# Kernel tuning notes

Hardware: AMD Instinct MI355X
Metric: run time of the kernel (lower is better)

The kernel has to match this reference:

```python
import jax, jax.numpy as jnp
import numpy as np

DIM = 512
HEADS = 8
DH = 64          # dim_head = 512 // 8
M = 256          # num_landmarks = 512 // 2
PINV_ITERS = 6
N_PATCH = 40000
IN_DIM = 1024
NUM_CLASSES = 2
GRID = 200       # ceil(sqrt(40000)) -> exact square, add_length = 0


def layernorm(x, w, b, eps=1e-5):
    mu = x.mean(-1, keepdims=True)
    var = ((x - mu) ** 2).mean(-1, keepdims=True)
    return (x - mu) * jax.lax.rsqrt(var + eps) * w + b


def moore_penrose_pinv(x, iters=PINV_ITERS):
    # lucidrains nystrom-attention iterative pseudoinverse
    ax = jnp.abs(x)
    z = jnp.swapaxes(x, -1, -2) / (jnp.max(ax.sum(-1)) * jnp.max(ax.sum(-2)))
    I = jnp.eye(x.shape[-1], dtype=x.dtype)
    for _ in range(iters):
        xz = x @ z
        z = 0.25 * z @ (13 * I - xz @ (15 * I - xz @ (7 * I - xz)))
    return z


def depthwise_conv2d(x, w, pad):
    # x: (B,C,H,W); w: (C,1,kh,kw) torch-style OIHW depthwise kernel
    return jax.lax.conv_general_dilated(
        x, w, (1, 1), [(pad[0], pad[0]), (pad[1], pad[1])],
        dimension_numbers=('NCHW', 'OIHW', 'NCHW'),
        feature_group_count=x.shape[1])


def nystrom_attention(x, qkv_w, out_w, out_b, res_w):
    b, n, _ = x.shape
    pad = (M - n % M) % M
    xp = jnp.pad(x, ((0, 0), (pad, 0), (0, 0)))   # pad at FRONT of sequence
    N = n + pad
    qkv = xp @ qkv_w                              # (b,N,3*h*d), no bias
    q, k, v = jnp.split(qkv, 3, axis=-1)
    to_heads = lambda t: t.reshape(b, N, HEADS, DH).transpose(0, 2, 1, 3)
    q, k, v = to_heads(q), to_heads(k), to_heads(v)
    q = q * (DH ** -0.5)
    l = N // M
    q_l = q.reshape(b, HEADS, M, l, DH).mean(axis=3)   # (b,h,m,d) landmarks
    k_l = k.reshape(b, HEADS, M, l, DH).mean(axis=3)
    attn1 = jax.nn.softmax(jnp.einsum('bhid,bhjd->bhij', q, k_l), axis=-1)   # (b,h,N,m)
    attn2 = jax.nn.softmax(jnp.einsum('bhid,bhjd->bhij', q_l, k_l), axis=-1)  # (b,h,m,m)
    attn3 = jax.nn.softmax(jnp.einsum('bhid,bhjd->bhij', q_l, k), axis=-1)   # (b,h,m,N)
    out = (attn1 @ moore_penrose_pinv(attn2)) @ (attn3 @ v)                   # (b,h,N,d)
    out = out + depthwise_conv2d(v, res_w, (16, 0))    # residual depthwise conv (kernel 33x1)
    out = out.transpose(0, 2, 1, 3).reshape(b, N, HEADS * DH)[:, -n:]
    return out @ out_w + out_b


def ppeg(x, w7, b7, w5, b5, w3, b3, H, W):
    B, _, C = x.shape
    cls_t, feat = x[:, :1], x[:, 1:]
    f = feat.transpose(0, 2, 1).reshape(B, C, H, W)
    y = (f
         + depthwise_conv2d(f, w7, (3, 3)) + b7[None, :, None, None]
         + depthwise_conv2d(f, w5, (2, 2)) + b5[None, :, None, None]
         + depthwise_conv2d(f, w3, (1, 1)) + b3[None, :, None, None])
    y = y.reshape(B, C, H * W).transpose(0, 2, 1)
    return jnp.concatenate([cls_t, y], axis=1)


def setup_inputs() -> dict:
    key = jax.random.key(0)
    ks = iter(jax.random.split(key, 32))
    r = lambda shape, s=0.02: jax.random.normal(next(ks), shape, dtype=jnp.float32) * s
    inp = {
        'x': jax.random.normal(next(ks), (1, N_PATCH, IN_DIM), dtype=jnp.float32),
        'fc1_w': r((IN_DIM, DIM)), 'fc1_b': jnp.zeros((DIM,), jnp.float32),
        'cls_token': r((1, 1, DIM), 1e-6),
        'l1_norm_w': jnp.ones((DIM,), jnp.float32), 'l1_norm_b': jnp.zeros((DIM,), jnp.float32),
        'l1_qkv_w': r((DIM, 3 * HEADS * DH)), 'l1_out_w': r((HEADS * DH, DIM)),
        'l1_out_b': jnp.zeros((DIM,), jnp.float32), 'l1_res_w': r((HEADS, 1, 33, 1)),
        'p7_w': r((DIM, 1, 7, 7)), 'p7_b': jnp.zeros((DIM,), jnp.float32),
        'p5_w': r((DIM, 1, 5, 5)), 'p5_b': jnp.zeros((DIM,), jnp.float32),
        'p3_w': r((DIM, 1, 3, 3)), 'p3_b': jnp.zeros((DIM,), jnp.float32),
        'l2_norm_w': jnp.ones((DIM,), jnp.float32), 'l2_norm_b': jnp.zeros((DIM,), jnp.float32),
        'l2_qkv_w': r((DIM, 3 * HEADS * DH)), 'l2_out_w': r((HEADS * DH, DIM)),
        'l2_out_b': jnp.zeros((DIM,), jnp.float32), 'l2_res_w': r((HEADS, 1, 33, 1)),
        'norm_w': jnp.ones((DIM,), jnp.float32), 'norm_b': jnp.zeros((DIM,), jnp.float32),
        'fc2_w': r((DIM, NUM_CLASSES)), 'fc2_b': jnp.zeros((NUM_CLASSES,), jnp.float32),
    }
    return inp


def reference(x, fc1_w, fc1_b, cls_token,
              l1_norm_w, l1_norm_b, l1_qkv_w, l1_out_w, l1_out_b, l1_res_w,
              p7_w, p7_b, p5_w, p5_b, p3_w, p3_b,
              l2_norm_w, l2_norm_b, l2_qkv_w, l2_out_w, l2_out_b, l2_res_w,
              norm_w, norm_b, fc2_w, fc2_b):
    # _fc1: Linear + ReLU (dropout inactive at eval)
    h = jax.nn.relu(x @ fc1_w + fc1_b)            # (1, 40000, 512)
    # 40000 = 200*200 -> add_length = 0, no square padding needed
    B = h.shape[0]
    h = jnp.concatenate([jnp.broadcast_to(cls_token, (B, 1, DIM)), h], axis=1)
    # layer1: pre-norm Nystrom attention with residual
    h = h + nystrom_attention(layernorm(h, l1_norm_w, l1_norm_b), l1_qkv_w, l1_out_w, l1_out_b, l1_res_w)
    # PPEG positional mixing on the 200x200 token grid
    h = ppeg(h, p7_w, p7_b, p5_w, p5_b, p3_w, p3_b, GRID, GRID)
    # layer2
    h = h + nystrom_attention(layernorm(h, l2_norm_w, l2_norm_b), l2_qkv_w, l2_out_w, l2_out_b, l2_res_w)
    h = layernorm(h, norm_w, norm_b)
    cls_out = h[:, 0]
    logits = cls_out @ fc2_w + fc2_b              # (1, num_classes)
    return logits
```

## Files before the change

### kernel.cpp

```cpp
#include <hip/hip_runtime.h>
#include <hip/hip_bf16.h>

#define DIMC   512
#define HEADS  8
#define DH     64
#define MLM    256
#define NPATCH 40000
#define NTOK   40001
#define PADF   191
#define NSEQ   40192
#define NSEQP  40224
#define LWIN   157
#define INDIM  1024
#define GRID   200
#define CHUNKS 64
#define PER    628

typedef _Float16 h8 __attribute__((ext_vector_type(8)));
typedef _Float16 h4 __attribute__((ext_vector_type(4)));
typedef float    f4 __attribute__((ext_vector_type(4)));
typedef float    f2 __attribute__((ext_vector_type(2)));

#define WAVE_LDS_FENCE() asm volatile("s_waitcnt lgkmcnt(0)" ::: "memory")

__device__ __forceinline__ void gl_lds(const _Float16* g, _Float16* l) {
  __builtin_amdgcn_global_load_lds(
      (const __attribute__((address_space(1))) void*)g,
      (__attribute__((address_space(3))) void*)l, 16, 0, 0);
}

template<int NW, bool ISMAX>
__device__ __forceinline__ float blkRed(float v, float* s) {
  #pragma unroll
  for (int o = 32; o; o >>= 1) {
    float t = __shfl_down(v, o, 64);
    v = ISMAX ? fmaxf(v, t) : v + t;
  }
  int lane = threadIdx.x & 63, w = threadIdx.x >> 6;
  __syncthreads();
  if (lane == 0) s[w] = v;
  __syncthreads();
  float r = s[0];
  #pragma unroll
  for (int i = 1; i < NW; i++) r = ISMAX ? fmaxf(r, s[i]) : r + s[i];
  return r;
}

__global__ __launch_bounds__(512)
void k_set_cls(const float* __restrict__ cls, float* __restrict__ h) {
  h[threadIdx.x] = cls[threadIdx.x];
}

__global__ __launch_bounds__(256)
void k_f32_to_f16(const float* __restrict__ in, _Float16* __restrict__ out) {
  int i = blockIdx.x * 256 + threadIdx.x;
  float4 v = ((const float4*)in)[i];
  h4 o = {(_Float16)v.x, (_Float16)v.y, (_Float16)v.z, (_Float16)v.w};
  *(h4*)(out + (size_t)i * 4) = o;
}

__global__ __launch_bounds__(256)
void k_zpad(_Float16* q16, _Float16* k16, _Float16* v16) {
  int idx = blockIdx.x * 256 + threadIdx.x;
  int h = idx >> 11, r = (idx >> 6) & 31, d = idx & 63;
  size_t a = ((size_t)h * NSEQP + NSEQ + r) * 64 + d;
  q16[a] = (_Float16)0.f; k16[a] = (_Float16)0.f; v16[a] = (_Float16)0.f;
}

__global__ __launch_bounds__(256)
void k_wt16(const float* __restrict__ B, _Float16* __restrict__ Bt, int K, int N)
{
  __shared__ float tile[32][33];
  int kb = blockIdx.x * 32, nb = blockIdx.y * 32;
  int x = threadIdx.x & 31, y0 = threadIdx.x >> 5;
  #pragma unroll
  for (int yy = y0; yy < 32; yy += 8)
    tile[yy][x] = B[(size_t)(kb + yy) * N + nb + x];
  __syncthreads();
  #pragma unroll
  for (int yy = y0; yy < 32; yy += 8)
    Bt[(size_t)(nb + yy) * K + kb + x] = (_Float16)tile[x][yy];
}

__global__ __launch_bounds__(256)
void k_gemm16(const _Float16* __restrict__ A, const _Float16* __restrict__ Bt,
              const float* __restrict__ bias, float* __restrict__ C,
              _Float16* __restrict__ q16, _Float16* __restrict__ k16, _Float16* __restrict__ v16,
              int Mr, int K, int N, int flags)
{
  __shared__ __attribute__((aligned(16))) _Float16 As[128 * 32];
  __shared__ __attribute__((aligned(16))) _Float16 Bs[128 * 32];
  int NT = N >> 7;
  int nwg = gridDim.x;
  int q8 = nwg >> 3, r8 = nwg & 7;
  int xcd = blockIdx.x & 7, sidx = blockIdx.x >> 3;
  int wgid = (xcd < r8) ? (xcd * (q8 + 1) + sidx)
                        : (r8 * (q8 + 1) + (xcd - r8) * q8 + sidx);
  int bm = (wgid / NT) * 128, bn = (wgid % NT) * 128;
  int t = threadIdx.x;
  int lane = t & 63, w = t >> 6;
  int wm = (w >> 1) * 64, wn = (w & 1) * 64;
  int r = lane & 15, q = lane >> 4;
  int sub = lane >> 2;
  int kq = (lane & 3) * 8;

  const f4 zero = {0.f, 0.f, 0.f, 0.f};
  f4 acc[4][4];
  #pragma unroll
  for (int mi = 0; mi < 4; mi++)
    #pragma unroll
    for (int nj = 0; nj < 4; nj++) acc[mi][nj] = zero;

  for (int k0 = 0; k0 < K; k0 += 32) {
    #pragma unroll
    for (int c = 0; c < 2; c++) {
      int rowA = (w * 2 + c) * 16 + sub;
      int gmA = bm + rowA; if (gmA > Mr - 1) gmA = Mr - 1;
      gl_lds(A  + (size_t)gmA * K + k0 + kq,          As + (w * 2 + c) * 512);
      gl_lds(Bt + (size_t)(bn + rowA) * K + k0 + kq,  Bs + (w * 2 + c) * 512);
    }
    __syncthreads();
    h8 af[4], bf[4];
    #pragma unroll
    for (int i = 0; i < 4; i++) {
      af[i] = *(const h8*)(As + (wm + i * 16 + r) * 32 + q * 8);
      bf[i] = *(const h8*)(Bs + (wn + i * 16 + r) * 32 + q * 8);
    }
    #pragma unroll
    for (int mi = 0; mi < 4; mi++)
      #pragma unroll
      for (int nj = 0; nj < 4; nj++)
        acc[mi][nj] = __builtin_amdgcn_mfma_f32_16x16x32_f16(bf[nj], af[mi], acc[mi][nj], 0, 0, 0);
    __syncthreads();
  }
  #pragma unroll
  for (int mi = 0; mi < 4; mi++) {
    int gm = bm + wm + mi * 16 + r;
    if (gm >= Mr) continue;
    #pragma unroll
    for (int nj = 0; nj < 4; nj++) {
      int gn = bn + wn + nj * 16 + q * 4;
      f4 v = acc[mi][nj];
      if (flags & 4) {
        int which = gn >> 9, hh = (gn >> 6) & 7, dd = gn & 63;
        _Float16* dst = (which == 0) ? q16 : (which == 1) ? k16 : v16;
        h4 o = {(_Float16)v[0], (_Float16)v[1], (_Float16)v[2], (_Float16)v[3]};
        *(h4*)(dst + ((size_t)hh * NSEQP + gm) * 64 + dd) = o;
      } else {
        if (bias) { f4 bv = *(const f4*)(bias + gn); v += bv; }
        float* cp = C + (size_t)gm * N + gn;
        if (flags & 2) { f4 cv = *(const f4*)cp; v += cv; }
        if (flags & 1) {
          v[0] = fmaxf(v[0], 0.f); v[1] = fmaxf(v[1], 0.f);
          v[2] = fmaxf(v[2], 0.f); v[3] = fmaxf(v[3], 0.f);
        }
        *(f4*)cp = v;
      }
    }
  }
}

__global__ __launch_bounds__(256)
void k_ln_pad(const float* __restrict__ h, const float* __restrict__ w,
              const float* __restrict__ b, _Float16* __restrict__ xln)
{
  __shared__ float sbuf[8];
  int t = blockIdx.x;
  int tid = threadIdx.x;
  _Float16* out = xln + (size_t)t * DIMC;
  if (t < PADF) { out[tid] = (_Float16)0.f; out[tid + 256] = (_Float16)0.f; return; }
  const float* row = h + (size_t)(t - PADF) * DIMC;
  float x0 = row[tid], x1 = row[tid + 256];
  float mu = blkRed<4,false>(x0 + x1, sbuf) * (1.f / 512.f);
  float d0 = x0 - mu, d1 = x1 - mu;
  float var = blkRed<4,false>(d0 * d0 + d1 * d1, sbuf) * (1.f / 512.f);
  float rstd = rsqrtf(var + 1e-5f);
  out[tid]       = (_Float16)(d0 * rstd * w[tid]       + b[tid]);
  out[tid + 256] = (_Float16)(d1 * rstd * w[tid + 256] + b[tid + 256]);
}

__global__ __launch_bounds__(256)
void k_vt(const _Float16* __restrict__ v16, _Float16* __restrict__ vt16)
{
  __shared__ _Float16 tl[64][72];
  int h = blockIdx.y;
  int t0 = blockIdx.x * 64;
  for (int c = threadIdx.x; c < 512; c += 256) {
    int row = c >> 3, ch = (c & 7) * 8;
    h8 v = {};
    if (t0 + row < NSEQP)
      v = *(const h8*)(v16 + ((size_t)h * NSEQP + t0 + row) * 64 + ch);
    *(h8*)&tl[row][ch] = v;
  }
  __syncthreads();
  int d = threadIdx.x & 63, tg = (threadIdx.x >> 6) * 16;
  if (t0 + tg < NSEQP) {
    _Float16 tmp[16];
    #pragma unroll
    for (int k = 0; k < 16; k++) tmp[k] = tl[tg + k][d];
    *(h8*)(vt16 + ((size_t)h * 64 + d) * NSEQP + t0 + tg)     = *(h8*)tmp;
    *(h8*)(vt16 + ((size_t)h * 64 + d) * NSEQP + t0 + tg + 8) = *(h8*)(tmp + 8);
  }
}

__global__ __launch_bounds__(256)
void k_landmarks(const _Float16* __restrict__ q16, const _Float16* __restrict__ k16,
                 float* __restrict__ ql, float* __restrict__ kl,
                 _Float16* __restrict__ ql16, _Float16* __restrict__ kl16)
{
  __shared__ float red[2][16][64];
  int h = blockIdx.x >> 8, i = blockIdx.x & 255;
  int jg = threadIdx.x >> 4, d4 = (threadIdx.x & 15) * 4;
  const _Float16* qb = q16 + ((size_t)h * NSEQP + i * LWIN) * 64;
  const _Float16* kb = k16 + ((size_t)h * NSEQP + i * LWIN) * 64;
  float sq[4] = {}, sk[4] = {};
  for (int j = jg; j < LWIN; j += 16) {
    h4 qv = *(const h4*)(qb + j * 64 + d4);
    h4 kv = *(const h4*)(kb + j * 64 + d4);
    #pragma unroll
    for (int c = 0; c < 4; c++) { sq[c] += (float)qv[c]; sk[c] += (float)kv[c]; }
  }
  #pragma unroll
  for (int c = 0; c < 4; c++) { red[0][jg][d4 + c] = sq[c]; red[1][jg][d4 + c] = sk[c]; }
  __syncthreads();
  if (threadIdx.x < 64) {
    int d = threadIdx.x;
    float aq = 0.f, ak = 0.f;
    #pragma unroll
    for (int g = 0; g < 16; g++) { aq += red[0][g][d]; ak += red[1][g][d]; }
    aq *= (0.125f / (float)LWIN);
    ak *= (1.f / (float)LWIN);
    size_t o = ((size_t)h * MLM + i) * DH + d;
    ql[o] = aq; kl[o] = ak;
    ql16[o] = (_Float16)aq;
    kl16[o] = (_Float16)(ak * 0.125f);
  }
}

__global__ __launch_bounds__(256)
void k_attn2(const float* __restrict__ ql, const float* __restrict__ kl, float* __restrict__ a2)
{
  __shared__ float qrow[DH];
  __shared__ float sbuf[8];
  int h = blockIdx.x >> 8, i = blockIdx.x & 255;
  int j = threadIdx.x;
  if (j < DH) qrow[j] = ql[(h * MLM + i) * DH + j];
  __syncthreads();
  const float* krow = kl + (size_t)(h * MLM + j) * DH;
  float s = 0.f;
  #pragma unroll 16
  for (int d = 0; d < DH; d++) s += qrow[d] * krow[d];
  float mx = blkRed<4,true>(s, sbuf);
  float e = __expf(s - mx);
  float sum = blkRed<4,false>(e, sbuf);
  a2[((size_t)h * MLM + i) * MLM + j] = e / sum;
}

__global__ __launch_bounds__(256)
void k_pinv_init1(const float* __restrict__ a2, float* __restrict__ hmax)
{
  __shared__ float sbuf[8];
  int h = blockIdx.x;
  int j = threadIdx.x;
  const float* A = a2 + (size_t)h * MLM * MLM;
  float cs = 0.f, rs = 0.f;
  for (int i = 0; i < MLM; i++) cs += A[i * MLM + j];
  for (int k = 0; k < MLM; k++) rs += A[j * MLM + k];
  float rmax = blkRed<4,true>(rs, sbuf);
  float cmax = blkRed<4,true>(cs, sbuf);
  if (j == 0) { hmax[h * 2] = rmax; hmax[h * 2 + 1] = cmax; }
}

__global__ __launch_bounds__(256)
void k_pinv_prep(const float* __restrict__ a2, const float* __restrict__ hmax,
                 _Float16* __restrict__ a2h, _Float16* __restrict__ a2l,
                 _Float16* __restrict__ zh,  _Float16* __restrict__ zl,
                 _Float16* __restrict__ zth, _Float16* __restrict__ ztl)
{
  __shared__ float tl[64][65];
  int h = blockIdx.x >> 4, tile = blockIdx.x & 15;
  int ti = (tile >> 2) * 64, tj = (tile & 3) * 64;
  float rm = 0.f, cm = 0.f;
  #pragma unroll
  for (int hh = 0; hh < HEADS; hh++) {
    rm = fmaxf(rm, hmax[2 * hh]);
    cm = fmaxf(cm, hmax[2 * hh + 1]);
  }
  float s = 1.f / (rm * cm);
  int row = threadIdx.x >> 4, c4 = (threadIdx.x & 15) * 4;
  #pragma unroll
  for (int rr = 0; rr < 4; rr++) {
    int rloc = rr * 16 + row;
    f4 v = *(const f4*)(a2 + ((size_t)h * MLM + ti + rloc) * MLM + tj + c4);
    h4 hi, lo, zhi, zlo;
    #pragma unroll
    for (int c = 0; c < 4; c++) {
      hi[c] = (_Float16)v[c];
      lo[c] = (_Float16)(v[c] - (float)hi[c]);
      float zv = v[c] * s;
      zhi[c] = (_Float16)zv;
      zlo[c] = (_Float16)(zv - (float)zhi[c]);
      tl[rloc][c4 + c] = zv;
    }
    size_t idx = ((size_t)h * MLM + ti + rloc) * MLM + tj + c4;
    *(h4*)(a2h + idx) = hi;  *(h4*)(a2l + idx) = lo;
    *(h4*)(zth + idx) = zhi; *(h4*)(ztl + idx) = zlo;
  }
  __syncthreads();
  #pragma unroll
  for (int rr = 0; rr < 4; rr++) {
    int rloc = rr * 16 + row;
    h4 hi, lo;
    #pragma unroll
    for (int c = 0; c < 4; c++) {
      float zv = tl[c4 + c][rloc];
      hi[c] = (_Float16)zv;
      lo[c] = (_Float16)(zv - (float)hi[c]);
    }
    size_t idx = ((size_t)h * MLM + tj + rloc) * MLM + ti + c4;
    *(h4*)(zh + idx) = hi; *(h4*)(zl + idx) = lo;
  }
}

__global__ __launch_bounds__(256)
void k_pbmm(const _Float16* __restrict__ Ah, const _Float16* __restrict__ Al,
            const _Float16* __restrict__ Bth, const _Float16* __restrict__ Btl,
            const _Float16* __restrict__ Eh, const _Float16* __restrict__ El,
            _Float16* __restrict__ Ch,  _Float16* __restrict__ Cl,
            _Float16* __restrict__ Cth, _Float16* __restrict__ Ctl,
            int N, float c0, float c1)
{
  __shared__ __attribute__((aligned(16))) _Float16 lds[16384];
  _Float16 *Ash = lds, *Asl = lds + 2048, *Bsh = lds + 4096, *Bsl = lds + 6144;
  _Float16 *Tt0 = lds + 8192, *Tt1 = lds + 12288;
  int tn = N >> 6;
  int bm = (blockIdx.x / tn) * 64, bn = (blockIdx.x % tn) * 64;
  int h = blockIdx.y;
  int tid = threadIdx.x, lane = tid & 63, w = tid >> 6;
  int wm = (w >> 1) * 32, wn = (w & 1) * 32;
  int r = lane & 15, q = lane >> 4;
  int sub = lane >> 2, kq = (lane & 3) * 8;

  const _Float16* Ahb = Ah + ((size_t)h * MLM + bm) * MLM;
  const _Float16* Alb = Al + ((size_t)h * MLM + bm) * MLM;
  const _Float16* Bhb = Bth + ((size_t)h * N + bn) * MLM;
  const _Float16* Blb = Btl + ((size_t)h * N + bn) * MLM;

  const f4 zero = {0.f, 0.f, 0.f, 0.f};
  f4 acc[2][2];
  #pragma unroll
  for (int mi = 0; mi < 2; mi++)
    #pragma unroll
    for (int nj = 0; nj < 2; nj++) acc[mi][nj] = zero;

  for (int k0 = 0; k0 < MLM; k0 += 32) {
    int rw = w * 16 + sub;
    gl_lds(Ahb + (size_t)rw * MLM + k0 + kq, Ash + w * 512);
    gl_lds(Alb + (size_t)rw * MLM + k0 + kq, Asl + w * 512);
    gl_lds(Bhb + (size_t)rw * MLM + k0 + kq, Bsh + w * 512);
    gl_lds(Blb + (size_t)rw * MLM + k0 + kq, Bsl + w * 512);
    __syncthreads();
    h8 afh[2], afl[2], bfh[2], bfl[2];
    #pragma unroll
    for (int i = 0; i < 2; i++) {
      afh[i] = *(const h8*)(Ash + (wm + i * 16 + r) * 32 + q * 8);
      afl[i] = *(const h8*)(Asl + (wm + i * 16 + r) * 32 + q * 8);
      bfh[i] = *(const h8*)(Bsh + (wn + i * 16 + r) * 32 + q * 8);
      bfl[i] = *(const h8*)(Bsl + (wn + i * 16 + r) * 32 + q * 8);
    }
    #pragma unroll
    for (int mi = 0; mi < 2; mi++)
      #pragma unroll
      for (int nj = 0; nj < 2; nj++) {
        acc[mi][nj] = __builtin_amdgcn_mfma_f32_16x16x32_f16(afh[mi], bfh[nj], acc[mi][nj], 0, 0, 0);
        acc[mi][nj] = __builtin_amdgcn_mfma_f32_16x16x32_f16(afh[mi], bfl[nj], acc[mi][nj], 0, 0, 0);
        acc[mi][nj] = __builtin_amdgcn_mfma_f32_16x16x32_f16(afl[mi], bfh[nj], acc[mi][nj], 0, 0, 0);
      }
    __syncthreads();
  }
  #pragma unroll
  for (int mi = 0; mi < 2; mi++) {
    #pragma unroll
    for (int i = 0; i < 4; i++) {
      int lm = wm + mi * 16 + q * 4 + i;
      #pragma unroll
      for (int nj = 0; nj < 2; nj++) {
        int ln = wn + nj * 16 + r;
        size_t ide = ((size_t)h * MLM + bm + lm) * N + bn + ln;
        float v = c0 * acc[mi][nj][i];
        if (Eh) v += c1 * ((float)Eh[ide] + (float)El[ide]);
        _Float16 hi = (_Float16)v;
        _Float16 lo = (_Float16)(v - (float)hi);
        if (Ch) { Ch[ide] = hi; Cl[ide] = lo; }
        int sw = lm ^ ((ln & 7) << 3);
        Tt0[ln * 64 + sw] = hi;
        Tt1[ln * 64 + sw] = lo;
      }
    }
  }
  __syncthreads();
  {
    int row = tid >> 2;
    int cb0 = (tid & 3) * 16;
    #pragma unroll
    for (int sg = 0; sg < 2; sg++) {
      int cb = cb0 + sg * 8;
      int swc = cb ^ ((row & 7) << 3);
      h8 vh = *(const h8*)(Tt0 + row * 64 + swc);
      h8 vl = *(const h8*)(Tt1 + row * 64 + swc);
      size_t idt = ((size_t)h * N + bn + row) * MLM + bm + cb;
      *(h8*)(Cth + idt) = vh;
      *(h8*)(Ctl + idt) = vl;
    }
  }
}

__global__ __launch_bounds__(256)
void k_attn3(const _Float16* __restrict__ ql16, const _Float16* __restrict__ k16,
             const _Float16* __restrict__ vt16,
             float* __restrict__ pm, float* __restrict__ ps, float* __restrict__ pacc)
{
  __shared__ __attribute__((aligned(16))) _Float16 Pl[4][64 * 40];
  int c = blockIdx.x, h = blockIdx.y;
  int tid = threadIdx.x, lane = tid & 63, w = tid >> 6;
  int r = lane & 15, q = lane >> 4;
  int t0 = c * PER;
  int m0 = w * 64;
  const _Float16* qlh = ql16 + (size_t)h * MLM * 64;
  const _Float16* kh  = k16  + (size_t)h * NSEQP * 64;
  const _Float16* vh  = vt16 + (size_t)h * 64 * NSEQP;
  _Float16* Pw = &Pl[w][0];

  h8 af[4][2];
  #pragma unroll
  for (int mt = 0; mt < 4; mt++)
    #pragma unroll
    for (int ks = 0; ks < 2; ks++)
      af[mt][ks] = *(const h8*)(qlh + (size_t)(m0 + mt * 16 + r) * 64 + ks * 32 + q * 8);

  const f4 zero = {0.f, 0.f, 0.f, 0.f};
  f4 acc[4][4];
  float mrun[4][4], lrun[4][4];
  #pragma unroll
  for (int mt = 0; mt < 4; mt++) {
    #pragma unroll
    for (int nd = 0; nd < 4; nd++) acc[mt][nd] = zero;
    #pragma unroll
    for (int i = 0; i < 4; i++) { mrun[mt][i] = -1e30f; lrun[mt][i] = 0.f; }
  }

  for (int tb = 0; tb < 20; tb++) {
    int tt = t0 + tb * 32;
    f4 S[4][2];
    #pragma unroll
    for (int mt = 0; mt < 4; mt++) { S[mt][0] = zero; S[mt][1] = zero; }
    #pragma unroll
    for (int nt = 0; nt < 2; nt++) {
      h8 b0 = *(const h8*)(kh + (size_t)(tt + nt * 16 + r) * 64 + q * 8);
      h8 b1 = *(const h8*)(kh + (size_t)(tt + nt * 16 + r) * 64 + 32 + q * 8);
      #pragma unroll
      for (int mt = 0; mt < 4; mt++) {
        S[mt][nt] = __builtin_amdgcn_mfma_f32_16x16x32_f16(af[mt][0], b0, S[mt][nt], 0, 0, 0);
        S[mt][nt] = __builtin_amdgcn_mfma_f32_16x16x32_f16(af[mt][1], b1, S[mt][nt], 0, 0, 0);
      }
    }
    if (tb == 19) {
      #pragma unroll
      for (int nt = 0; nt < 2; nt++) {
        bool valid = (tb * 32 + nt * 16 + r) < PER;
        #pragma unroll
        for (int mt = 0; mt < 4; mt++)
          #pragma unroll
          for (int i = 0; i < 4; i++)
            S[mt][nt][i] = valid ? S[mt][nt][i] : -1e30f;
      }
    }
    #pragma unroll
    for (int mt = 0; mt < 4; mt++) {
      bool tg = false;
      #pragma unroll
      for (int i = 0; i < 4; i++)
        tg = tg || (S[mt][0][i] > mrun[mt][i] + 8.f) || (S[mt][1][i] > mrun[mt][i] + 8.f);
      if (__any(tg)) {
        float nm[4], al[4];
        #pragma unroll
        for (int i = 0; i < 4; i++) {
          nm[i] = fmaxf(S[mt][0][i], S[mt][1][i]);
          #pragma unroll
          for (int o = 1; o < 16; o <<= 1) nm[i] = fmaxf(nm[i], __shfl_xor(nm[i], o, 64));
          nm[i] = fmaxf(nm[i], mrun[mt][i]);
          al[i] = __expf(mrun[mt][i] - nm[i]);
          mrun[mt][i] = nm[i];
          lrun[mt][i] *= al[i];
        }
        #pragma unroll
        for (int nd = 0; nd < 4; nd++)
          #pragma unroll
          for (int i = 0; i < 4; i++) acc[mt][nd][i] *= al[i];
      }
      #pragma unroll
      for (int i = 0; i < 4; i++) {
        float p0 = __expf(S[mt][0][i] - mrun[mt][i]);
        float p1 = __expf(S[mt][1][i] - mrun[mt][i]);
        lrun[mt][i] += p0 + p1;
        S[mt][0][i] = p0; S[mt][1][i] = p1;
      }
      #pragma unroll
      for (int nt = 0; nt < 2; nt++)
        #pragma unroll
        for (int i = 0; i < 4; i++)
          Pw[(mt * 16 + q * 4 + i) * 40 + nt * 16 + r] = (_Float16)S[mt][nt][i];
    }
    WAVE_LDS_FENCE();
    h8 bv[4];
    #pragma unroll
    for (int nd = 0; nd < 4; nd++)
      bv[nd] = *(const h8*)(vh + (size_t)(nd * 16 + r) * NSEQP + tt + q * 8);
    #pragma unroll
    for (int mt = 0; mt < 4; mt++) {
      h8 ap = *(const h8*)(Pw + (mt * 16 + r) * 40 + q * 8);
      #pragma unroll
      for (int nd = 0; nd < 4; nd++)
        acc[mt][nd] = __builtin_amdgcn_mfma_f32_16x16x32_f16(ap, bv[nd], acc[mt][nd], 0, 0, 0);
    }
    WAVE_LDS_FENCE();
  }
  #pragma unroll
  for (int mt = 0; mt < 4; mt++)
    #pragma unroll
    for (int i = 0; i < 4; i++)
      #pragma unroll
      for (int o = 1; o < 16; o <<= 1) lrun[mt][i] += __shfl_xor(lrun[mt][i], o, 64);
  int cidx = h * CHUNKS + c;
  #pragma unroll
  for (int mt = 0; mt < 4; mt++) {
    int rowb = m0 + mt * 16 + q * 4;
    if (r == 0) {
      #pragma unroll
      for (int i = 0; i < 4; i++) {
        pm[(size_t)cidx * MLM + rowb + i] = mrun[mt][i];
        ps[(size_t)cidx * MLM + rowb + i] = lrun[mt][i];
      }
    }
    #pragma unroll
    for (int nd = 0; nd < 4; nd++)
      #pragma unroll
      for (int i = 0; i < 4; i++)
        pacc[((size_t)cidx * MLM + rowb + i) * 64 + nd * 16 + r] = acc[mt][nd][i];
  }
}

__global__ __launch_bounds__(64)
void k_attn3_reduce(const float* __restrict__ pm, const float* __restrict__ ps,
                    const float* __restrict__ pacc,
                    _Float16* __restrict__ avth, _Float16* __restrict__ avtl)
{
  int h = blockIdx.x >> 8, i = blockIdx.x & 255;
  int d = threadIdx.x;
  float m = -1e30f;
  for (int c = 0; c < CHUNKS; c++) m = fmaxf(m, pm[(h * CHUNKS + c) * MLM + i]);
  float l = 0.f, a = 0.f;
  for (int c = 0; c < CHUNKS; c++) {
    int idx = (h * CHUNKS + c) * MLM + i;
    float w = __expf(pm[idx] - m);
    l += ps[idx] * w;
    a += pacc[(size_t)idx * DH + d] * w;
  }
  float v = a / l;
  _Float16 hi = (_Float16)v;
  size_t o = ((size_t)h * DH + d) * MLM + i;
  avth[o] = hi;
  avtl[o] = (_Float16)(v - (float)hi);
}

__global__ __launch_bounds__(256)
void k_conv(const _Float16* __restrict__ v16, const float* __restrict__ rw,
            _Float16* __restrict__ xat)
{
  __shared__ float tl[160][64];
  int h = blockIdx.y;
  int t0 = PADF + blockIdx.x * 128;
  for (int c = threadIdx.x; c < 160 * 16; c += 256) {
    int row = c >> 4, d4 = (c & 15) * 4;
    int ts = t0 - 16 + row;
    f4 val = {0.f, 0.f, 0.f, 0.f};
    if (ts >= 0 && ts < NSEQ) {
      h4 hv = *(const h4*)(v16 + ((size_t)h * NSEQP + ts) * 64 + d4);
      val[0] = (float)hv[0]; val[1] = (float)hv[1]; val[2] = (float)hv[2]; val[3] = (float)hv[3];
    }
    *(f4*)&tl[row][d4] = val;
  }
  __syncthreads();
  float wt[33];
  #pragma unroll
  for (int tap = 0; tap < 33; tap++) wt[tap] = rw[h * 33 + tap];
  int d4 = (threadIdx.x & 15) * 4, r0 = threadIdx.x >> 4;
  #pragma unroll
  for (int k = 0; k < 8; k++) {
    int r = k * 16 + r0;
    int t = t0 + r;
    f4 acc = {0.f, 0.f, 0.f, 0.f};
    #pragma unroll
    for (int tap = 0; tap < 33; tap++) {
      f4 vv = *(const f4*)&tl[r + tap][d4];
      acc[0] += wt[tap] * vv[0]; acc[1] += wt[tap] * vv[1];
      acc[2] += wt[tap] * vv[2]; acc[3] += wt[tap] * vv[3];
    }
    if (t < NSEQ) {
      h4 o = {(_Float16)acc[0], (_Float16)acc[1], (_Float16)acc[2], (_Float16)acc[3]};
      *(h4*)(xat + (size_t)t * DIMC + h * 64 + d4) = o;
    }
  }
}

__global__ __launch_bounds__(256)
void k_attn1(const _Float16* __restrict__ q16, const _Float16* __restrict__ kl16,
             const _Float16* __restrict__ w2t16, _Float16* __restrict__ xat)
{
  __shared__ __attribute__((aligned(16))) _Float16 Pl[4][64 * 40];
  int h = blockIdx.y;
  int t0 = blockIdx.x * 256;
  int tid = threadIdx.x, lane = tid & 63, w = tid >> 6;
  int r = lane & 15, q = lane >> 4;
  int m0 = w * 64;
  const _Float16* qh  = q16  + (size_t)h * NSEQP * 64;
  const _Float16* klh = kl16 + (size_t)h * MLM * 64;
  const _Float16* w2h = w2t16 + (size_t)h * 64 * 256;
  _Float16* Pw = &Pl[w][0];

  h8 af[4][2];
  #pragma unroll
  for (int mt = 0; mt < 4; mt++)
    #pragma unroll
    for (int ks = 0; ks < 2; ks++)
      af[mt][ks] = *(const h8*)(qh + (size_t)(t0 + m0 + mt * 16 + r) * 64 + ks * 32 + q * 8);

  const f4 zero = {0.f, 0.f, 0.f, 0.f};
  f4 acc[4][4];
  float mrun[4][4], lrun[4][4];
  #pragma unroll
  for (int mt = 0; mt < 4; mt++) {
    #pragma unroll
    for (int nd = 0; nd < 4; nd++) acc[mt][nd] = zero;
    #pragma unroll
    for (int i = 0; i < 4; i++) { mrun[mt][i] = -1e30f; lrun[mt][i] = 0.f; }
  }

  for (int tb = 0; tb < 8; tb++) {
    int tt = tb * 32;
    f4 S[4][2];
    #pragma unroll
    for (int mt = 0; mt < 4; mt++) { S[mt][0] = zero; S[mt][1] = zero; }
    #pragma unroll
    for (int nt = 0; nt < 2; nt++) {
      h8 b0 = *(const h8*)(klh + (size_t)(tt + nt * 16 + r) * 64 + q * 8);
      h8 b1 = *(const h8*)(klh + (size_t)(tt + nt * 16 + r) * 64 + 32 + q * 8);
      #pragma unroll
      for (int mt = 0; mt < 4; mt++) {
        S[mt][nt] = __builtin_amdgcn_mfma_f32_16x16x32_f16(af[mt][0], b0, S[mt][nt], 0, 0, 0);
        S[mt][nt] = __builtin_amdgcn_mfma_f32_16x16x32_f16(af[mt][1], b1, S[mt][nt], 0, 0, 0);
      }
    }
    #pragma unroll
    for (int mt = 0; mt < 4; mt++) {
      bool tg = false;
      #pragma unroll
      for (int i = 0; i < 4; i++)
        tg = tg || (S[mt][0][i] > mrun[mt][i] + 8.f) || (S[mt][1][i] > mrun[mt][i] + 8.f);
      if (__any(tg)) {
        float nm[4], al[4];
        #pragma unroll
        for (int i = 0; i < 4; i++) {
          nm[i] = fmaxf(S[mt][0][i], S[mt][1][i]);
          #pragma unroll
          for (int o = 1; o < 16; o <<= 1) nm[i] = fmaxf(nm[i], __shfl_xor(nm[i], o, 64));
          nm[i] = fmaxf(nm[i], mrun[mt][i]);
          al[i] = __expf(mrun[mt][i] - nm[i]);
          mrun[mt][i] = nm[i];
          lrun[mt][i] *= al[i];
        }
        #pragma unroll
        for (int nd = 0; nd < 4; nd++)
          #pragma unroll
          for (int i = 0; i < 4; i++) acc[mt][nd][i] *= al[i];
      }
      #pragma unroll
      for (int i = 0; i < 4; i++) {
        float p0 = __expf(S[mt][0][i] - mrun[mt][i]);
        float p1 = __expf(S[mt][1][i] - mrun[mt][i]);
        lrun[mt][i] += p0 + p1;
        S[mt][0][i] = p0; S[mt][1][i] = p1;
      }
      #pragma unroll
      for (int nt = 0; nt < 2; nt++)
        #pragma unroll
        for (int i = 0; i < 4; i++)
          Pw[(mt * 16 + q * 4 + i) * 40 + nt * 16 + r] = (_Float16)S[mt][nt][i];
    }
    WAVE_LDS_FENCE();
    h8 bw[4];
    #pragma unroll
    for (int nd = 0; nd < 4; nd++)
      bw[nd] = *(const h8*)(w2h + (size_t)(nd * 16 + r) * 256 + tt + q * 8);
    #pragma unroll
    for (int mt = 0; mt < 4; mt++) {
      h8 ap = *(const h8*)(Pw + (mt * 16 + r) * 40 + q * 8);
      #pragma unroll
      for (int nd = 0; nd < 4; nd++)
        acc[mt][nd] = __builtin_amdgcn_mfma_f32_16x16x32_f16(ap, bw[nd], acc[mt][nd], 0, 0, 0);
    }
    WAVE_LDS_FENCE();
  }
  #pragma unroll
  for (int mt = 0; mt < 4; mt++)
    #pragma unroll
    for (int i = 0; i < 4; i++)
      #pragma unroll
      for (int o = 1; o < 16; o <<= 1) lrun[mt][i] += __shfl_xor(lrun[mt][i], o, 64);
  #pragma unroll
  for (int half = 0; half < 2; half++) {
    #pragma unroll
    for (int mt2 = 0; mt2 < 2; mt2++) {
      int mt = half * 2 + mt2;
      float li[4];
      #pragma unroll
      for (int i = 0; i < 4; i++) li[i] = 1.f / lrun[mt][i];
      #pragma unroll
      for (int nd = 0; nd < 4; nd++)
        #pragma unroll
        for (int i = 0; i < 4; i++)
          Pw[(mt2 * 16 + q * 4 + i) * 72 + nd * 16 + r] = (_Float16)(acc[mt][nd][i] * li[i]);
    }
    WAVE_LDS_FENCE();
    #pragma unroll
    for (int c = 0; c < 4; c++) {
      int row = c * 8 + (lane >> 3);
      int ch = (lane & 7) * 8;
      int t = t0 + m0 + half * 32 + row;
      if (t >= PADF) {
        _Float16* dst = xat + (size_t)t * DIMC + h * 64 + ch;
        h8 cv = *(h8*)dst;
        h8 pv = *(const h8*)(Pw + row * 72 + ch);
        h8 o;
        #pragma unroll
        for (int k = 0; k < 8; k++) o[k] = (_Float16)((float)cv[k] + (float)pv[k]);
        *(h8*)dst = o;
      }
    }
    WAVE_LDS_FENCE();
  }
}

__global__ __launch_bounds__(256)
void k_transpose_fw(const float* __restrict__ h, float* __restrict__ g)
{
  __shared__ float tile[32][33];
  int pb = blockIdx.x * 32, cb = blockIdx.y * 32;
  int x = threadIdx.x & 31, y0 = threadIdx.x >> 5;
  #pragma unroll
  for (int yy = y0; yy < 32; yy += 8)
    tile[yy][x] = h[(size_t)(1 + pb + yy) * DIMC + cb + x];
  __syncthreads();
  #pragma unroll
  for (int yy = y0; yy < 32; yy += 8)
    g[(size_t)(cb + yy) * NPATCH + pb + x] = tile[x][yy];
}

__global__ __launch_bounds__(256)
void k_ppeg(const float* __restrict__ g,
            const float* __restrict__ w7, const float* __restrict__ b7,
            const float* __restrict__ w5, const float* __restrict__ b5,
            const float* __restrict__ w3, const float* __restrict__ b3,
            float* __restrict__ o)
{
  __shared__ f2 tl[38][40];
  int cp = blockIdx.y;
  int c0 = cp * 2, c1 = c0 + 1;
  int ty0 = (blockIdx.x / 7) * 32, tx0 = (blockIdx.x % 7) * 32;
  const float* g0 = g + (size_t)c0 * NPATCH;
  const float* g1 = g + (size_t)c1 * NPATCH;
  for (int e = threadIdx.x; e < 38 * 40; e += 256) {
    int row = e / 40, col = e % 40;
    int y = ty0 - 3 + row, x = tx0 - 3 + col;
    f2 v = {0.f, 0.f};
    if (y >= 0 && y < GRID && x >= 0 && x < GRID && col < 38) {
      v[0] = g0[y * GRID + x];
      v[1] = g1[y * GRID + x];
    }
    tl[row][col] = v;
  }
  __syncthreads();
  int tx4 = (threadIdx.x & 7) * 4, ty = threadIdx.x >> 3;
  f2 bb = {b7[c0] + b5[c0] + b3[c0], b7[c1] + b5[c1] + b3[c1]};
  f2 acc[4];
  #pragma unroll
  for (int j = 0; j < 4; j++) acc[j] = bb + tl[ty + 3][tx4 + 3 + j];
  #pragma unroll
  for (int ky = 0; ky < 7; ky++) {
    f2 f[10];
    #pragma unroll
    for (int k = 0; k < 5; k++)
      *(f4*)&f[k * 2] = *(const f4*)&tl[ty + ky][tx4 + k * 2];
    #pragma unroll
    for (int kx = 0; kx < 7; kx++) {
      f2 wv = {w7[c0 * 49 + ky * 7 + kx], w7[c1 * 49 + ky * 7 + kx]};
      #pragma unroll
      for (int j = 0; j < 4; j++) acc[j] += wv * f[kx + j];
    }
    if (ky >= 1 && ky <= 5) {
      #pragma unroll
      for (int kx = 0; kx < 5; kx++) {
        f2 wv = {w5[c0 * 25 + (ky - 1) * 5 + kx], w5[c1 * 25 + (ky - 1) * 5 + kx]};
        #pragma unroll
        for (int j = 0; j < 4; j++) acc[j] += wv * f[1 + kx + j];
      }
    }
    if (ky >= 2 && ky <= 4) {
      #pragma unroll
      for (int kx = 0; kx < 3; kx++) {
        f2 wv = {w3[c0 * 9 + (ky - 2) * 3 + kx], w3[c1 * 9 + (ky - 2) * 3 + kx]};
        #pragma unroll
        for (int j = 0; j < 4; j++) acc[j] += wv * f[2 + kx + j];
      }
    }
  }
  int y = ty0 + ty, xb = tx0 + tx4;
  if (y < GRID && xb < GRID) {
    f4 o0 = {acc[0][0], acc[1][0], acc[2][0], acc[3][0]};
    f4 o1 = {acc[0][1], acc[1][1], acc[2][1], acc[3][1]};
    *(f4*)(o + (size_t)c0 * NPATCH + y * GRID + xb) = o0;
    *(f4*)(o + (size_t)c1 * NPATCH + y * GRID + xb) = o1;
  }
}

__global__ __launch_bounds__(256)
void k_transpose_bw(const float* __restrict__ g, float* __restrict__ h)
{
  __shared__ float tile[32][33];
  int pb = blockIdx.x * 32, cb = blockIdx.y * 32;
  int x = threadIdx.x & 31, y0 = threadIdx.x >> 5;
  #pragma unroll
  for (int yy = y0; yy < 32; yy += 8)
    tile[yy][x] = g[(size_t)(cb + yy) * NPATCH + pb + x];
  __syncthreads();
  #pragma unroll
  for (int yy = y0; yy < 32; yy += 8)
    h[(size_t)(1 + pb + yy) * DIMC + cb + x] = tile[x][yy];
}

__global__ __launch_bounds__(512)
void k_final(const float* __restrict__ h, const float* __restrict__ nw, const float* __restrict__ nb,
             const float* __restrict__ fw, const float* __restrict__ fb, float* __restrict__ out)
{
  __shared__ float sbuf[8];
  int d = threadIdx.x;
  float x = h[d];
  float mu = blkRed<8,false>(x, sbuf) * (1.f / 512.f);
  float dd = x - mu;
  float var = blkRed<8,false>(dd * dd, sbuf) * (1.f / 512.f);
  float cls = dd * rsqrtf(var + 1e-5f) * nw[d] + nb[d];
  float l0 = blkRed<8,false>(cls * fw[d * 2 + 0], sbuf);
  float l1 = blkRed<8,false>(cls * fw[d * 2 + 1], sbuf);
  if (d == 0) { out[0] = l0 + fb[0]; out[1] = l1 + fb[1]; }
}

struct Pair4 { _Float16 *h, *l, *th, *tl; };
struct WsPtrs {
  float *h, *ql, *kl, *a2, *hmax, *scal, *pm, *ps, *pacc;
  _Float16 *xat16, *q16, *k16, *v16, *vt16, *ql16, *kl16, *x16;
  _Float16 *a2h, *a2l, *avth, *avtl;
  Pair4 zA, zB, xz, u, u2, w2;
};

static void attention_layer(const WsPtrs& P,
                            const float* nw, const float* nb, const _Float16* qkvw16,
                            const _Float16* ow16, const float* ob, const float* rw,
                            hipStream_t stream)
{
  k_zpad<<<64, 256, 0, stream>>>(P.q16, P.k16, P.v16);
  k_ln_pad<<<NSEQ, 256, 0, stream>>>(P.h, nw, nb, P.xat16);
  k_gemm16<<<dim3((NSEQ / 128) * (1536 / 128)), 256, 0, stream>>>(
      P.xat16, qkvw16, nullptr, nullptr, P.q16, P.k16, P.v16, NSEQ, DIMC, 3 * DIMC, 4);
  k_vt<<<dim3(629, HEADS), 256, 0, stream>>>(P.v16, P.vt16);
  k_landmarks<<<HEADS * MLM, 256, 0, stream>>>(P.q16, P.k16, P.ql, P.kl, P.ql16, P.kl16);
  k_attn2<<<HEADS * MLM, 256, 0, stream>>>(P.ql, P.kl, P.a2);
  k_pinv_init1<<<HEADS, 256, 0, stream>>>(P.a2, P.hmax);
  k_pinv_prep<<<HEADS * 16, 256, 0, stream>>>(P.a2, P.hmax,
      P.a2h, P.a2l, P.zA.h, P.zA.l, P.zA.th, P.zA.tl);
  Pair4 z = P.zA, zn = P.zB;
  for (int it = 0; it < 6; it++) {
    k_pbmm<<<dim3(16, HEADS), 256, 0, stream>>>(P.a2h, P.a2l, z.th, z.tl,
        nullptr, nullptr, P.xz.h, P.xz.l, P.xz.th, P.xz.tl, MLM, 1.f, 0.f);
    k_pbmm<<<dim3(16, HEADS), 256, 0, stream>>>(P.xz.h, P.xz.l, P.xz.th, P.xz.tl,
        P.xz.h, P.xz.l, nullptr, nullptr, P.u.th, P.u.tl, MLM, -1.f, 7.f);
    k_pbmm<<<dim3(16, HEADS), 256, 0, stream>>>(P.xz.h, P.xz.l, P.u.th, P.u.tl,
        P.xz.h, P.xz.l, nullptr, nullptr, P.u2.th, P.u2.tl, MLM, -1.f, 15.f);
    k_pbmm<<<dim3(16, HEADS), 256, 0, stream>>>(z.h, z.l, P.u2.th, P.u2.tl,
        z.h, z.l, zn.h, zn.l, zn.th, zn.tl, MLM, -0.25f, 3.25f);
    Pair4 t = z; z = zn; zn = t;
  }
  k_attn3<<<dim3(CHUNKS, HEADS), 256, 0, stream>>>(P.ql16, P.k16, P.vt16, P.pm, P.ps, P.pacc);
  k_attn3_reduce<<<HEADS * MLM, 64, 0, stream>>>(P.pm, P.ps, P.pacc, P.avth, P.avtl);
  k_pbmm<<<dim3(4, HEADS), 256, 0, stream>>>(z.h, z.l, P.avth, P.avtl,
      nullptr, nullptr, nullptr, nullptr, P.w2.th, P.w2.tl, DH, 1.f, 0.f);
  k_conv<<<dim3(313, HEADS), 256, 0, stream>>>(P.v16, rw, P.xat16);
  k_attn1<<<dim3(157, HEADS), 256, 0, stream>>>(P.q16, P.kl16, P.w2.th, P.xat16);
  k_gemm16<<<dim3(((NTOK + 127) / 128) * (DIMC / 128)), 256, 0, stream>>>(
      P.xat16 + (size_t)PADF * DIMC, ow16, ob, P.h, nullptr, nullptr, nullptr, NTOK, DIMC, DIMC, 2);
}

extern "C" void kernel_launch(void* const* d_in, const int* in_sizes, int n_in,
                              void* d_out, int out_size, void* d_ws, size_t ws_size,
                              hipStream_t stream)
{
  const float* x      = (const float*)d_in[0];
  const float* fc1_w  = (const float*)d_in[1];
  const float* fc1_b  = (const float*)d_in[2];
  const float* cls    = (const float*)d_in[3];
  const float* l1_nw  = (const float*)d_in[4];
  const float* l1_nb  = (const float*)d_in[5];
  const float* l1_qkv = (const float*)d_in[6];
  const float* l1_ow  = (const float*)d_in[7];
  const float* l1_ob  = (const float*)d_in[8];
  const float* l1_rw  = (const float*)d_in[9];
  const float* p7w    = (const float*)d_in[10];
  const float* p7b    = (const float*)d_in[11];
  const float* p5w    = (const float*)d_in[12];
  const float* p5b    = (const float*)d_in[13];
  const float* p3w    = (const float*)d_in[14];
  const float* p3b    = (const float*)d_in[15];
  const float* l2_nw  = (const float*)d_in[16];
  const float* l2_nb  = (const float*)d_in[17];
  const float* l2_qkv = (const float*)d_in[18];
  const float* l2_ow  = (const float*)d_in[19];
  const float* l2_ob  = (const float*)d_in[20];
  const float* l2_rw  = (const float*)d_in[21];
  const float* nw     = (const float*)d_in[22];
  const float* nb     = (const float*)d_in[23];
  const float* fc2w   = (const float*)d_in[24];
  const float* fc2b   = (const float*)d_in[25];
  float* out = (float*)d_out;

  float* W = (float*)d_ws;
  WsPtrs P;
  size_t off = 0;
  P.h     = W + off;               off += 20480512ull;
  P.xat16 = (_Float16*)(W + off);  off += 10289152ull;
  float* R0 = W + off;
  P.q16   = (_Float16*)R0;
  P.k16   = P.q16 + 20594688ull;
  P.v16   = P.k16 + 20594688ull;
  P.vt16  = P.v16 + 20594688ull;
  P.x16   = P.q16;
  off += 41189376ull;
  P.ql    = W + off; off += 131072;
  P.kl    = W + off; off += 131072;
  P.ql16  = (_Float16*)(W + off); off += 65536;
  P.kl16  = (_Float16*)(W + off); off += 65536;
  P.a2    = W + off; off += 524288;
  _Float16* HP = (_Float16*)(W + off);
  size_t ho = 0;
  P.a2h = HP + ho; ho += 524288; P.a2l = HP + ho; ho += 524288;
  auto alloc4 = [&](Pair4& p, size_t n) {
    p.h = HP + ho; ho += n; p.l = HP + ho; ho += n;
    p.th = HP + ho; ho += n; p.tl = HP + ho; ho += n;
  };
  alloc4(P.zA, 524288); alloc4(P.zB, 524288); alloc4(P.xz, 524288);
  alloc4(P.u, 524288);  alloc4(P.u2, 524288);
  alloc4(P.w2, 131072);
  P.avth = HP + ho; ho += 131072; P.avtl = HP + ho; ho += 131072;
  off += (ho + 1) / 2;
  P.hmax  = W + off; P.scal = P.hmax + 16; off += 32;
  P.pm    = W + off; off += 131072;
  P.ps    = W + off; off += 131072;
  P.pacc  = W + off; off += 8388608;
  _Float16* fc1t  = (_Float16*)(W + off);
  _Float16* qkv1t = fc1t  + 524288;
  _Float16* out1t = qkv1t + 786432;
  _Float16* qkv2t = out1t + 262144;
  _Float16* out2t = qkv2t + 786432;

  k_wt16<<<dim3(INDIM / 32, DIMC / 32), 256, 0, stream>>>(fc1_w, fc1t, INDIM, DIMC);
  k_wt16<<<dim3(DIMC / 32, 1536 / 32), 256, 0, stream>>>(l1_qkv, qkv1t, DIMC, 1536);
  k_wt16<<<dim3(DIMC / 32, DIMC / 32), 256, 0, stream>>>(l1_ow, out1t, DIMC, DIMC);
  k_wt16<<<dim3(DIMC / 32, 1536 / 32), 256, 0, stream>>>(l2_qkv, qkv2t, DIMC, 1536);
  k_wt16<<<dim3(DIMC / 32, DIMC / 32), 256, 0, stream>>>(l2_ow, out2t, DIMC, DIMC);

  k_f32_to_f16<<<NPATCH * INDIM / 1024, 256, 0, stream>>>(x, P.x16);
  k_gemm16<<<dim3(((NPATCH + 127) / 128) * (DIMC / 128)), 256, 0, stream>>>(
      P.x16, fc1t, fc1_b, P.h + DIMC, nullptr, nullptr, nullptr, NPATCH, INDIM, DIMC, 1);
  k_set_cls<<<1, 512, 0, stream>>>(cls, P.h);

  attention_layer(P, l1_nw, l1_nb, qkv1t, out1t, l1_ob, l1_rw, stream);

  float* fgrid = R0;
  float* cout  = R0 + 20480000ull;
  k_transpose_fw<<<dim3(NPATCH / 32, DIMC / 32), 256, 0, stream>>>(P.h, fgrid);
  k_ppeg<<<dim3(7 * 7, DIMC / 2), 256, 0, stream>>>(fgrid, p7w, p7b, p5w, p5b, p3w, p3b, cout);
  k_transpose_bw<<<dim3(NPATCH / 32, DIMC / 32), 256, 0, stream>>>(cout, P.h);

  attention_layer(P, l2_nw, l2_nb, qkv2t, out2t, l2_ob, l2_rw, stream);

  k_final<<<1, 512, 0, stream>>>(P.h, nw, nb, fc2w, fc2b, out);
}
```

Baseline: 2.146 ms.

## Restructure pinv matmul into single-wave 32x64 tiles with double-buffered LDS

New measurement: 2.196 ms. +2.3%, slower.

```diff
diff --git a/kernel.cpp b/kernel.cpp
--- a/kernel.cpp
+++ b/kernel.cpp
@@ -322,7 +322,7 @@
   }
 }
 
-__global__ __launch_bounds__(256)
+__global__ __launch_bounds__(64)
 void k_pbmm(const _Float16* __restrict__ Ah, const _Float16* __restrict__ Al,
             const _Float16* __restrict__ Bth, const _Float16* __restrict__ Btl,
             const _Float16* __restrict__ Eh, const _Float16* __restrict__ El,
@@ -330,14 +330,13 @@
             _Float16* __restrict__ Cth, _Float16* __restrict__ Ctl,
             int N, float c0, float c1)
 {
-  __shared__ __attribute__((aligned(16))) _Float16 lds[16384];
-  _Float16 *Ash = lds, *Asl = lds + 2048, *Bsh = lds + 4096, *Bsl = lds + 6144;
-  _Float16 *Tt0 = lds + 8192, *Tt1 = lds + 12288;
+  __shared__ __attribute__((aligned(16))) _Float16 lds[2][6144];
   int tn = N >> 6;
-  int bm = (blockIdx.x / tn) * 64, bn = (blockIdx.x % tn) * 64;
-  int h = blockIdx.y;
-  int tid = threadIdx.x, lane = tid & 63, w = tid >> 6;
-  int wm = (w >> 1) * 32, wn = (w & 1) * 32;
+  int tph = 8 * tn;
+  int b = blockIdx.x;
+  int h = b / tph, tile = b % tph;
+  int bm = (tile / tn) * 32, bn = (tile % tn) * 64;
+  int lane = threadIdx.x;
   int r = lane & 15, q = lane >> 4;
   int sub = lane >> 2, kq = (lane & 3) * 8;
 
@@ -347,67 +346,92 @@
   const _Float16* Blb = Btl + ((size_t)h * N + bn) * MLM;
 
   const f4 zero = {0.f, 0.f, 0.f, 0.f};
-  f4 acc[2][2];
+  f4 acc[2][4];
   #pragma unroll
   for (int mi = 0; mi < 2; mi++)
     #pragma unroll
-    for (int nj = 0; nj < 2; nj++) acc[mi][nj] = zero;
-
-  for (int k0 = 0; k0 < MLM; k0 += 32) {
-    int rw = w * 16 + sub;
-    gl_lds(Ahb + (size_t)rw * MLM + k0 + kq, Ash + w * 512);
-    gl_lds(Alb + (size_t)rw * MLM + k0 + kq, Asl + w * 512);
-    gl_lds(Bhb + (size_t)rw * MLM + k0 + kq, Bsh + w * 512);
-    gl_lds(Blb + (size_t)rw * MLM + k0 + kq, Bsl + w * 512);
-    __syncthreads();
-    h8 afh[2], afl[2], bfh[2], bfl[2];
+    for (int nj = 0; nj < 4; nj++) acc[mi][nj] = zero;
+
+  auto stage = [&](int buf, int k0) {
+    _Float16* L = &lds[buf][0];
+    gl_lds(Ahb + (size_t)sub * MLM + k0 + kq,        L);
+    gl_lds(Ahb + (size_t)(16 + sub) * MLM + k0 + kq, L + 512);
+    gl_lds(Alb + (size_t)sub * MLM + k0 + kq,        L + 1024);
+    gl_lds(Alb + (size_t)(16 + sub) * MLM + k0 + kq, L + 1536);
+    #pragma unroll
+    for (int c = 0; c < 4; c++)
+      gl_lds(Bhb + (size_t)(c * 16 + sub) * MLM + k0 + kq, L + 2048 + c * 512);
+    #pragma unroll
+    for (int c = 0; c < 4; c++)
+      gl_lds(Blb + (size_t)(c * 16 + sub) * MLM + k0 + kq, L + 4096 + c * 512);
+  };
+
+  stage(0, 0);
+  for (int s = 0; s < 8; s++) {
+    int cur = s & 1;
+    if (s < 7) {
+      WAVE_LDS_FENCE();
+      stage(1 - cur, (s + 1) * 32);
+      asm volatile("s_waitcnt vmcnt(12)" ::: "memory");
+    } else {
+      asm volatile("s_waitcnt vmcnt(0)" ::: "memory");
+    }
+    _Float16* L = &lds[cur][0];
+    h8 afh[2], afl[2], bfh[4], bfl[4];
     #pragma unroll
     for (int i = 0; i < 2; i++) {
-      afh[i] = *(const h8*)(Ash + (wm + i * 16 + r) * 32 + q * 8);
-      afl[i] = *(const h8*)(Asl + (wm + i * 16 + r) * 32 + q * 8);
-      bfh[i] = *(const h8*)(Bsh + (wn + i * 16 + r) * 32 + q * 8);
-      bfl[i] = *(const h8*)(Bsl + (wn + i * 16 + r) * 32 + q * 8);
+      afh[i] = *(const h8*)(L + (i * 16 + r) * 32 + q * 8);
+      afl[i] = *(const h8*)(L + 1024 + (i * 16 + r) * 32 + q * 8);
+    }
+    #pragma unroll
+    for (int j = 0; j < 4; j++) {
+      bfh[j] = *(const h8*)(L + 2048 + (j * 16 + r) * 32 + q * 8);
+      bfl[j] = *(const h8*)(L + 4096 + (j * 16 + r) * 32 + q * 8);
     }
     #pragma unroll
     for (int mi = 0; mi < 2; mi++)
       #pragma unroll
-      for (int nj = 0; nj < 2; nj++) {
+      for (int nj = 0; nj < 4; nj++) {
         acc[mi][nj] = __builtin_amdgcn_mfma_f32_16x16x32_f16(afh[mi], bfh[nj], acc[mi][nj], 0, 0, 0);
         acc[mi][nj] = __builtin_amdgcn_mfma_f32_16x16x32_f16(afh[mi], bfl[nj], acc[mi][nj], 0, 0, 0);
         acc[mi][nj] = __builtin_amdgcn_mfma_f32_16x16x32_f16(afl[mi], bfh[nj], acc[mi][nj], 0, 0, 0);
       }
-    __syncthreads();
-  }
+  }
+  WAVE_LDS_FENCE();
+  _Float16* Tt0 = &lds[0][0];
+  _Float16* Tt1 = &lds[0][2048];
   #pragma unroll
   for (int mi = 0; mi < 2; mi++) {
     #pragma unroll
-    for (int i = 0; i < 4; i++) {
-      int lm = wm + mi * 16 + q * 4 + i;
-      #pragma unroll
-      for (int nj = 0; nj < 2; nj++) {
-        int ln = wn + nj * 16 + r;
+    for (int nj = 0; nj < 4; nj++) {
+      int ln = nj * 16 + r;
+      int X = (ln & 3) << 3;
+      h4 hv, lv;
+      #pragma unroll
+      for (int i = 0; i < 4; i++) {
+        int lm = mi * 16 + q * 4 + i;
         size_t ide = ((size_t)h * MLM + bm + lm) * N + bn + ln;
         float v = c0 * acc[mi][nj][i];
         if (Eh) v += c1 * ((float)Eh[ide] + (float)El[ide]);
         _Float16 hi = (_Float16)v;
         _Float16 lo = (_Float16)(v - (float)hi);
         if (Ch) { Ch[ide] = hi; Cl[ide] = lo; }
-        int sw = lm ^ ((ln & 7) << 3);
-        Tt0[ln * 64 + sw] = hi;
-        Tt1[ln * 64 + sw] = lo;
-      }
-    }
-  }
-  __syncthreads();
+        hv[i] = hi; lv[i] = lo;
+      }
+      int swb = (mi * 16 + q * 4) ^ X;
+      *(h4*)(Tt0 + ln * 32 + swb) = hv;
+      *(h4*)(Tt1 + ln * 32 + swb) = lv;
+    }
+  }
+  WAVE_LDS_FENCE();
   {
-    int row = tid >> 2;
-    int cb0 = (tid & 3) * 16;
-    #pragma unroll
-    for (int sg = 0; sg < 2; sg++) {
-      int cb = cb0 + sg * 8;
-      int swc = cb ^ ((row & 7) << 3);
-      h8 vh = *(const h8*)(Tt0 + row * 64 + swc);
-      h8 vl = *(const h8*)(Tt1 + row * 64 + swc);
+    int row = lane;
+    #pragma unroll
+    for (int cbk = 0; cbk < 4; cbk++) {
+      int cb = cbk * 8;
+      int swc = cb ^ ((row & 3) << 3);
+      h8 vh = *(const h8*)(Tt0 + row * 32 + swc);
+      h8 vl = *(const h8*)(Tt1 + row * 32 + swc);
       size_t idt = ((size_t)h * N + bn + row) * MLM + bm + cb;
       *(h8*)(Cth + idt) = vh;
       *(h8*)(Ctl + idt) = vl;
@@ -889,19 +913,19 @@
       P.a2h, P.a2l, P.zA.h, P.zA.l, P.zA.th, P.zA.tl);
   Pair4 z = P.zA, zn = P.zB;
   for (int it = 0; it < 6; it++) {
-    k_pbmm<<<dim3(16, HEADS), 256, 0, stream>>>(P.a2h, P.a2l, z.th, z.tl,
+    k_pbmm<<<dim3(HEADS * 8 * (MLM >> 6)), 64, 0, stream>>>(P.a2h, P.a2l, z.th, z.tl,
         nullptr, nullptr, P.xz.h, P.xz.l, P.xz.th, P.xz.tl, MLM, 1.f, 0.f);
-    k_pbmm<<<dim3(16, HEADS), 256, 0, stream>>>(P.xz.h, P.xz.l, P.xz.th, P.xz.tl,
+    k_pbmm<<<dim3(HEADS * 8 * (MLM >> 6)), 64, 0, stream>>>(P.xz.h, P.xz.l, P.xz.th, P.xz.tl,
         P.xz.h, P.xz.l, nullptr, nullptr, P.u.th, P.u.tl, MLM, -1.f, 7.f);
-    k_pbmm<<<dim3(16, HEADS), 256, 0, stream>>>(P.xz.h, P.xz.l, P.u.th, P.u.tl,
+    k_pbmm<<<dim3(HEADS * 8 * (MLM >> 6)), 64, 0, stream>>>(P.xz.h, P.xz.l, P.u.th, P.u.tl,
         P.xz.h, P.xz.l, nullptr, nullptr, P.u2.th, P.u2.tl, MLM, -1.f, 15.f);
-    k_pbmm<<<dim3(16, HEADS), 256, 0, stream>>>(z.h, z.l, P.u2.th, P.u2.tl,
+    k_pbmm<<<dim3(HEADS * 8 * (MLM >> 6)), 64, 0, stream>>>(z.h, z.l, P.u2.th, P.u2.tl,
         z.h, z.l, zn.h, zn.l, zn.th, zn.tl, MLM, -0.25f, 3.25f);
     Pair4 t = z; z = zn; zn = t;
   }
   k_attn3<<<dim3(CHUNKS, HEADS), 256, 0, stream>>>(P.ql16, P.k16, P.vt16, P.pm, P.ps, P.pacc);
   k_attn3_reduce<<<HEADS * MLM, 64, 0, stream>>>(P.pm, P.ps, P.pacc, P.avth, P.avtl);
-  k_pbmm<<<dim3(4, HEADS), 256, 0, stream>>>(z.h, z.l, P.avth, P.avtl,
+  k_pbmm<<<dim3(HEADS * 8 * (DH >> 6)), 64, 0, stream>>>(z.h, z.l, P.avth, P.avtl,
       nullptr, nullptr, nullptr, nullptr, P.w2.th, P.w2.tl, DH, 1.f, 0.f);
   k_conv<<<dim3(313, HEADS), 256, 0, stream>>>(P.v16, rw, P.xat16);
   k_attn1<<<dim3(157, HEADS), 256, 0, stream>>>(P.q16, P.kl16, P.w2.th, P.xat16);
```
